# Optimization experiments

Measured on AMD Instinct MI355X. Metric: run time of the kernel, lower is better.

Reference implementation:

```python
import jax, jax.numpy as jnp
import numpy as np

TEMPERATURE = 0.07


def setup_inputs() -> dict:
    key = jax.random.key(0)
    k1, k2 = jax.random.split(key)
    B, D = 8192, 1024
    emb1 = jax.random.normal(k1, (B, D), dtype=jnp.float32)
    emb2 = jax.random.normal(k2, (B, D), dtype=jnp.float32)
    return {"emb1": emb1, "emb2": emb2}


def reference(emb1, emb2):
    B = emb1.shape[0]
    # [B, B] similarity logits scaled by temperature
    logits = jnp.matmul(emb1, emb2.T) / TEMPERATURE
    # SigLIP-style contrastive loss: diagonal entries are positives,
    # off-diagonal entries are negatives.
    # positive: -logsigmoid(logits) on diag; negative: -logsigmoid(-logits) off-diag
    pos = -jax.nn.log_sigmoid(jnp.diagonal(logits))            # [B]
    neg = -jax.nn.log_sigmoid(-logits)                          # [B, B]
    # negative_mask zeroes the diagonal -> subtract diagonal contribution
    neg_sum = neg.sum() - jnp.sum(jnp.diagonal(neg))
    loss = (pos.sum() + neg_sum) / B
    return loss
```

## Files before the change

### kernel.cpp

```cpp
#include <hip/hip_runtime.h>


#define B_DIM 8192
#define K_DIM 1024
#define BM 256
#define BN 128
#define BKB 128
#define NT (K_DIM / BKB)
#define ABRICK 32768
#define BBRICK 16384
#define BUFSZ 49152

typedef int i32x4 __attribute__((ext_vector_type(4)));
typedef int i32x8 __attribute__((ext_vector_type(8)));
typedef float f32x4 __attribute__((ext_vector_type(4)));

template <int PANEL>
__device__ __forceinline__ void brick_store(const float* __restrict__ in,
                                            unsigned char* __restrict__ out,
                                            float scale, int i) {
  constexpr int BRICK = PANEL * 128;
  const int o = i * 16;
  const int b = o / BRICK;
  const int p = b >> 3, t = b & 7;
  const int w = o & (BRICK - 1);
  const int fb = w >> 11;
  const int h = (w >> 10) & 1;
  const int kch = (w >> 8) & 3;
  const int lr = (w >> 4) & 15;
  const int row = p * PANEL + fb * 16 + lr;
  const int kb = t * 128 + kch * 32 + h * 16;
  const float4* src = (const float4*)(in + (size_t)row * K_DIM + kb);
  float4 v0 = src[0], v1 = src[1], v2 = src[2], v3 = src[3];
  unsigned w0 = 0, w1 = 0, w2 = 0, w3 = 0;
  w0 = __builtin_amdgcn_cvt_pk_fp8_f32(v0.x * scale, v0.y * scale, w0, 0);
  w0 = __builtin_amdgcn_cvt_pk_fp8_f32(v0.z * scale, v0.w * scale, w0, 1);
  w1 = __builtin_amdgcn_cvt_pk_fp8_f32(v1.x * scale, v1.y * scale, w1, 0);
  w1 = __builtin_amdgcn_cvt_pk_fp8_f32(v1.z * scale, v1.w * scale, w1, 1);
  w2 = __builtin_amdgcn_cvt_pk_fp8_f32(v2.x * scale, v2.y * scale, w2, 0);
  w2 = __builtin_amdgcn_cvt_pk_fp8_f32(v2.z * scale, v2.w * scale, w2, 1);
  w3 = __builtin_amdgcn_cvt_pk_fp8_f32(v3.x * scale, v3.y * scale, w3, 0);
  w3 = __builtin_amdgcn_cvt_pk_fp8_f32(v3.z * scale, v3.w * scale, w3, 1);
  *(uint4*)(out + o) = make_uint4(w0, w1, w2, w3);
}

__global__ __launch_bounds__(256) void cvt_fused(
    const float* __restrict__ e1, const float* __restrict__ e2,
    unsigned char* __restrict__ A8, unsigned char* __restrict__ B8,
    int nbA, float scaleA) {
  const int blk = blockIdx.x;
  if (blk < nbA)
    brick_store<BM>(e1, A8, scaleA, blk * 256 + threadIdx.x);
  else
    brick_store<BN>(e2, B8, 1.0f, (blk - nbA) * 256 + threadIdx.x);
}

template <bool DIAG>
__device__ __forceinline__ float softplus_sum(const f32x4 (&acc)[4][4],
                                              int rbase, int cbase) {
  float lin = 0.f, cor = 0.f;
#pragma unroll
  for (int m = 0; m < 4; ++m) {
#pragma unroll
    for (int n = 0; n < 4; ++n) {
#pragma unroll
      for (int r = 0; r < 4; ++r) {
        float x = acc[m][n][r];
        if (DIAG) {
          int row = rbase + m * 16 + r;
          int col = cbase + n * 16;
          if (row == col) x = -x;
        }
        lin += fmaxf(x, 0.f);
        cor += __logf(1.f + __expf(-fabsf(x)));
      }
    }
  }
  return lin + cor;
}

#define STAGEA(SB, J, TI)                                                     \
  __builtin_amdgcn_global_load_lds(                                           \
      (const __attribute__((address_space(1))) void*)(const void*)(           \
          srcA + (TI) * ABRICK + (J) * 8192),                                 \
      (__attribute__((address_space(3))) void*)(void*)(                       \
          lds + (SB) + dA + (J) * 8192),                                      \
      16, 0, 0)
#define STAGEB(SB, J, TI)                                                     \
  __builtin_amdgcn_global_load_lds(                                           \
      (const __attribute__((address_space(1))) void*)(const void*)(           \
          srcB + (TI) * BBRICK + (J) * 8192),                                 \
      (__attribute__((address_space(3))) void*)(void*)(                       \
          lds + (SB) + dB + (J) * 8192),                                      \
      16, 0, 0)

#define LDA(OUT, RB, M)                                                       \
  {                                                                           \
    const unsigned char* _b =                                                 \
        ldsL + ((RB) + ((wr * 4 + (M)) << 11));                               \
    i32x4 _lo = *(const i32x4*)(_b);                                          \
    i32x4 _hi = *(const i32x4*)(_b + 1024);                                   \
    OUT = __builtin_shufflevector(_lo, _hi, 0, 1, 2, 3, 4, 5, 6, 7);          \
  }
#define LDB(OUT, RB, N)                                                       \
  {                                                                           \
    const unsigned char* _b =                                                 \
        ldsL + ((RB) + 32768 + ((wc * 4 + (N)) << 11));                       \
    i32x4 _lo = *(const i32x4*)(_b);                                          \
    i32x4 _hi = *(const i32x4*)(_b + 1024);                                   \
    OUT = __builtin_shufflevector(_lo, _hi, 0, 1, 2, 3, 4, 5, 6, 7);          \
  }

#define MFMA(AF, BF, M, N)                                                    \
  acc[M][N] = __builtin_amdgcn_mfma_scale_f32_16x16x128_f8f6f4(               \
      AF, BF, acc[M][N], 0, 0, 0, 127, 0, 127)

__global__ __launch_bounds__(512, 1) void siglip_gemm(
    const unsigned char* __restrict__ A8,
    const unsigned char* __restrict__ B8,
    float* __restrict__ partials) {
  __shared__ unsigned char lds[3 * BUFSZ];
  __shared__ float wsum[8];

  const int tid = threadIdx.x;
  const int wave = tid >> 6;
  const int lane = tid & 63;
  const int wr = wave >> 1;
  const int wc = wave & 1;
  const int brow = blockIdx.y;
  const int bcol = blockIdx.x;

  f32x4 acc[4][4];
#pragma unroll
  for (int m = 0; m < 4; ++m)
#pragma unroll
    for (int n = 0; n < 4; ++n) acc[m][n] = f32x4{0.f, 0.f, 0.f, 0.f};

  const unsigned char* srcA =
      A8 + (size_t)brow * (NT * ABRICK) + wave * 1024 + (lane << 4);
  const unsigned char* srcB =
      B8 + (size_t)bcol * (NT * BBRICK) + wave * 1024 + (lane << 4);
  const int dA = wave * 1024;
  const int dB = 32768 + wave * 1024;
  const unsigned char* ldsL = lds + (lane << 4);

  STAGEA(0, 0, 0); STAGEA(0, 1, 0); STAGEA(0, 2, 0); STAGEA(0, 3, 0);
  STAGEB(0, 0, 0); STAGEB(0, 1, 0);
  STAGEA(BUFSZ, 0, 1); STAGEA(BUFSZ, 1, 1);
  STAGEA(BUFSZ, 2, 1); STAGEA(BUFSZ, 3, 1);
  STAGEB(BUFSZ, 0, 1); STAGEB(BUFSZ, 1, 1);
  asm volatile("s_waitcnt vmcnt(6)" ::: "memory");
  __builtin_amdgcn_s_barrier();
  __builtin_amdgcn_sched_barrier(0);

#pragma unroll
  for (int T = 0; T < NT; ++T) {
    const int rb = (T % 3) * BUFSZ;
    const int sb = ((T + 2) % 3) * BUFSZ;

    i32x8 b0, b1, b2, b3, a0, a1, a2, a3;
    LDB(b0, rb, 0); LDB(b1, rb, 1); LDB(b2, rb, 2); LDB(b3, rb, 3);
    LDA(a0, rb, 0); LDA(a1, rb, 1); LDA(a2, rb, 2); LDA(a3, rb, 3);

    if (T < NT - 2) {
      STAGEA(sb, 0, T + 2); STAGEA(sb, 1, T + 2);
      STAGEA(sb, 2, T + 2); STAGEA(sb, 3, T + 2);
      STAGEB(sb, 0, T + 2); STAGEB(sb, 1, T + 2);
      asm volatile("s_waitcnt vmcnt(6)" ::: "memory");
    } else if (T == NT - 2) {
      asm volatile("s_waitcnt vmcnt(0)" ::: "memory");
    }

    __builtin_amdgcn_s_setprio(1);
    MFMA(a0, b0, 0, 0); MFMA(a0, b1, 0, 1); MFMA(a0, b2, 0, 2); MFMA(a0, b3, 0, 3);
    MFMA(a1, b0, 1, 0); MFMA(a1, b1, 1, 1); MFMA(a1, b2, 1, 2); MFMA(a1, b3, 1, 3);
    MFMA(a2, b0, 2, 0); MFMA(a2, b1, 2, 1); MFMA(a2, b2, 2, 2); MFMA(a2, b3, 2, 3);
    MFMA(a3, b0, 3, 0); MFMA(a3, b1, 3, 1); MFMA(a3, b2, 3, 2); MFMA(a3, b3, 3, 3);
    __builtin_amdgcn_s_setprio(0);

    __builtin_amdgcn_s_barrier();
    __builtin_amdgcn_sched_barrier(0);
  }

  const int rbase = brow * BM + wr * 64 + (lane >> 4) * 4;
  const int cbase = bcol * BN + wc * 64 + (lane & 15);
  float lsum;
  if ((bcol >> 1) == brow)
    lsum = softplus_sum<true>(acc, rbase, cbase);
  else
    lsum = softplus_sum<false>(acc, rbase, cbase);

#pragma unroll
  for (int off = 32; off > 0; off >>= 1) lsum += __shfl_down(lsum, off);
  if (lane == 0) wsum[wave] = lsum;
  __syncthreads();
  if (tid == 0) {
    float s = 0.f;
#pragma unroll
    for (int w = 0; w < 8; ++w) s += wsum[w];
    partials[blockIdx.y * gridDim.x + blockIdx.x] = s;
  }
}

__global__ void reduce_kernel(const float* __restrict__ partials, int n,
                              float* __restrict__ out) {
  __shared__ float s[256];
  float v = 0.f;
  for (int i = threadIdx.x; i < n; i += 256) v += partials[i];
  s[threadIdx.x] = v;
  __syncthreads();
  for (int off = 128; off > 0; off >>= 1) {
    if ((int)threadIdx.x < off) s[threadIdx.x] += s[threadIdx.x + off];
    __syncthreads();
  }
  if (threadIdx.x == 0) out[0] = s[0] / (float)B_DIM;
}

extern "C" void kernel_launch(void* const* d_in, const int* in_sizes, int n_in,
                              void* d_out, int out_size, void* d_ws, size_t ws_size,
                              hipStream_t stream) {
  const float* emb1 = (const float*)d_in[0];
  const float* emb2 = (const float*)d_in[1];

  unsigned char* A8 = (unsigned char*)d_ws;
  unsigned char* B8 = A8 + (size_t)B_DIM * K_DIM;
  float* partials = (float*)(B8 + (size_t)B_DIM * K_DIM);

  const float INV_T = 1.0f / 0.07f;
  const int nbA = (B_DIM * K_DIM / 16) / 256;
  cvt_fused<<<2 * nbA, 256, 0, stream>>>(emb1, emb2, A8, B8, nbA, INV_T);

  dim3 grid(B_DIM / BN, B_DIM / BM);
  siglip_gemm<<<grid, 512, 0, stream>>>(A8, B8, partials);

  const int nparts = (B_DIM / BM) * (B_DIM / BN);
  reduce_kernel<<<1, 256, 0, stream>>>(partials, nparts, (float*)d_out);
}
```

Before: 119.5 us.

## Switch GEMM to 128x128 tiles, 4 waves, double buffering, two blocks per CU

Shrinks the GEMM block tile from 256x128 with 8 waves and triple-buffered LDS to 128x128 with 4 waves and double-buffered LDS, so two blocks can share a CU. The FP8 brick layout for both operands becomes a single 128-row panel. The aim is to overlap one block's memory waits with another block's compute instead of relying on a deeper per-block prefetch. In exchange, each A byte is loaded from global memory twice as often, the prefetch depth drops to one stage with a full vmcnt(0) wait every iteration, and the grid and partials count double.

```diff
diff --git a/kernel.cpp b/kernel.cpp
--- a/kernel.cpp
+++ b/kernel.cpp
@@ -3,32 +3,29 @@
 
 #define B_DIM 8192
 #define K_DIM 1024
-#define BM 256
-#define BN 128
+#define BT 128
 #define BKB 128
 #define NT (K_DIM / BKB)
-#define ABRICK 32768
-#define BBRICK 16384
-#define BUFSZ 49152
+#define BRICK 16384
+#define PANEL_BYTES (NT * BRICK)
+#define BUFSZ 32768
 
 typedef int i32x4 __attribute__((ext_vector_type(4)));
 typedef int i32x8 __attribute__((ext_vector_type(8)));
 typedef float f32x4 __attribute__((ext_vector_type(4)));
 
-template <int PANEL>
 __device__ __forceinline__ void brick_store(const float* __restrict__ in,
                                             unsigned char* __restrict__ out,
                                             float scale, int i) {
-  constexpr int BRICK = PANEL * 128;
   const int o = i * 16;
-  const int b = o / BRICK;
+  const int b = o >> 14;
   const int p = b >> 3, t = b & 7;
   const int w = o & (BRICK - 1);
   const int fb = w >> 11;
   const int h = (w >> 10) & 1;
   const int kch = (w >> 8) & 3;
   const int lr = (w >> 4) & 15;
-  const int row = p * PANEL + fb * 16 + lr;
+  const int row = p * 128 + fb * 16 + lr;
   const int kb = t * 128 + kch * 32 + h * 16;
   const float4* src = (const float4*)(in + (size_t)row * K_DIM + kb);
   float4 v0 = src[0], v1 = src[1], v2 = src[2], v3 = src[3];
@@ -50,9 +47,9 @@
     int nbA, float scaleA) {
   const int blk = blockIdx.x;
   if (blk < nbA)
-    brick_store<BM>(e1, A8, scaleA, blk * 256 + threadIdx.x);
+    brick_store(e1, A8, scaleA, blk * 256 + threadIdx.x);
   else
-    brick_store<BN>(e2, B8, 1.0f, (blk - nbA) * 256 + threadIdx.x);
+    brick_store(e2, B8, 1.0f, (blk - nbA) * 256 + threadIdx.x);
 }
 
 template <bool DIAG>
@@ -79,33 +76,31 @@
   return lin + cor;
 }
 
-#define STAGEA(SB, J, TI)                                                     \
+#define STAGEA(SB, Q, TI)                                                     \
   __builtin_amdgcn_global_load_lds(                                           \
       (const __attribute__((address_space(1))) void*)(const void*)(           \
-          srcA + (TI) * ABRICK + (J) * 8192),                                 \
+          srcA + (TI) * BRICK + (Q) * 1024),                                  \
       (__attribute__((address_space(3))) void*)(void*)(                       \
-          lds + (SB) + dA + (J) * 8192),                                      \
+          lds + (SB) + dA + (Q) * 1024),                                      \
       16, 0, 0)
-#define STAGEB(SB, J, TI)                                                     \
+#define STAGEB(SB, Q, TI)                                                     \
   __builtin_amdgcn_global_load_lds(                                           \
       (const __attribute__((address_space(1))) void*)(const void*)(           \
-          srcB + (TI) * BBRICK + (J) * 8192),                                 \
+          srcB + (TI) * BRICK + (Q) * 1024),                                  \
       (__attribute__((address_space(3))) void*)(void*)(                       \
-          lds + (SB) + dB + (J) * 8192),                                      \
+          lds + (SB) + dB + (Q) * 1024),                                      \
       16, 0, 0)
 
 #define LDA(OUT, RB, M)                                                       \
   {                                                                           \
-    const unsigned char* _b =                                                 \
-        ldsL + ((RB) + ((wr * 4 + (M)) << 11));                               \
+    const unsigned char* _b = ldsL + ((RB) + ((wr * 4 + (M)) << 11));         \
     i32x4 _lo = *(const i32x4*)(_b);                                          \
     i32x4 _hi = *(const i32x4*)(_b + 1024);                                   \
     OUT = __builtin_shufflevector(_lo, _hi, 0, 1, 2, 3, 4, 5, 6, 7);          \
   }
 #define LDB(OUT, RB, N)                                                       \
   {                                                                           \
-    const unsigned char* _b =                                                 \
-        ldsL + ((RB) + 32768 + ((wc * 4 + (N)) << 11));                       \
+    const unsigned char* _b = ldsL + ((RB) + 16384 + ((wc * 4 + (N)) << 11)); \
     i32x4 _lo = *(const i32x4*)(_b);                                          \
     i32x4 _hi = *(const i32x4*)(_b + 1024);                                   \
     OUT = __builtin_shufflevector(_lo, _hi, 0, 1, 2, 3, 4, 5, 6, 7);          \
@@ -115,12 +110,12 @@
   acc[M][N] = __builtin_amdgcn_mfma_scale_f32_16x16x128_f8f6f4(               \
       AF, BF, acc[M][N], 0, 0, 0, 127, 0, 127)
 
-__global__ __launch_bounds__(512, 1) void siglip_gemm(
+__global__ __launch_bounds__(256, 2) void siglip_gemm(
     const unsigned char* __restrict__ A8,
     const unsigned char* __restrict__ B8,
     float* __restrict__ partials) {
-  __shared__ unsigned char lds[3 * BUFSZ];
-  __shared__ float wsum[8];
+  __shared__ unsigned char lds[2 * BUFSZ];
+  __shared__ float wsum[4];
 
   const int tid = threadIdx.x;
   const int wave = tid >> 6;
@@ -137,39 +132,35 @@
     for (int n = 0; n < 4; ++n) acc[m][n] = f32x4{0.f, 0.f, 0.f, 0.f};
 
   const unsigned char* srcA =
-      A8 + (size_t)brow * (NT * ABRICK) + wave * 1024 + (lane << 4);
+      A8 + (size_t)brow * PANEL_BYTES + wave * 4096 + (lane << 4);
   const unsigned char* srcB =
-      B8 + (size_t)bcol * (NT * BBRICK) + wave * 1024 + (lane << 4);
-  const int dA = wave * 1024;
-  const int dB = 32768 + wave * 1024;
+      B8 + (size_t)bcol * PANEL_BYTES + wave * 4096 + (lane << 4);
+  const int dA = wave * 4096;
+  const int dB = 16384 + wave * 4096;
   const unsigned char* ldsL = lds + (lane << 4);
 
   STAGEA(0, 0, 0); STAGEA(0, 1, 0); STAGEA(0, 2, 0); STAGEA(0, 3, 0);
-  STAGEB(0, 0, 0); STAGEB(0, 1, 0);
-  STAGEA(BUFSZ, 0, 1); STAGEA(BUFSZ, 1, 1);
-  STAGEA(BUFSZ, 2, 1); STAGEA(BUFSZ, 3, 1);
-  STAGEB(BUFSZ, 0, 1); STAGEB(BUFSZ, 1, 1);
-  asm volatile("s_waitcnt vmcnt(6)" ::: "memory");
+  STAGEB(0, 0, 0); STAGEB(0, 1, 0); STAGEB(0, 2, 0); STAGEB(0, 3, 0);
+  asm volatile("s_waitcnt vmcnt(0)" ::: "memory");
   __builtin_amdgcn_s_barrier();
   __builtin_amdgcn_sched_barrier(0);
 
 #pragma unroll
   for (int T = 0; T < NT; ++T) {
-    const int rb = (T % 3) * BUFSZ;
-    const int sb = ((T + 2) % 3) * BUFSZ;
+    const int rb = (T & 1) * BUFSZ;
+    const int sb = rb ^ BUFSZ;
 
     i32x8 b0, b1, b2, b3, a0, a1, a2, a3;
     LDB(b0, rb, 0); LDB(b1, rb, 1); LDB(b2, rb, 2); LDB(b3, rb, 3);
     LDA(a0, rb, 0); LDA(a1, rb, 1); LDA(a2, rb, 2); LDA(a3, rb, 3);
 
-    if (T < NT - 2) {
-      STAGEA(sb, 0, T + 2); STAGEA(sb, 1, T + 2);
-      STAGEA(sb, 2, T + 2); STAGEA(sb, 3, T + 2);
-      STAGEB(sb, 0, T + 2); STAGEB(sb, 1, T + 2);
-      asm volatile("s_waitcnt vmcnt(6)" ::: "memory");
-    } else if (T == NT - 2) {
-      asm volatile("s_waitcnt vmcnt(0)" ::: "memory");
+    if (T < NT - 1) {
+      STAGEA(sb, 0, T + 1); STAGEA(sb, 1, T + 1);
+      STAGEA(sb, 2, T + 1); STAGEA(sb, 3, T + 1);
+      STAGEB(sb, 0, T + 1); STAGEB(sb, 1, T + 1);
+      STAGEB(sb, 2, T + 1); STAGEB(sb, 3, T + 1);
     }
+    __builtin_amdgcn_sched_barrier(0);
 
     __builtin_amdgcn_s_setprio(1);
     MFMA(a0, b0, 0, 0); MFMA(a0, b1, 0, 1); MFMA(a0, b2, 0, 2); MFMA(a0, b3, 0, 3);
@@ -178,28 +169,29 @@
     MFMA(a3, b0, 3, 0); MFMA(a3, b1, 3, 1); MFMA(a3, b2, 3, 2); MFMA(a3, b3, 3, 3);
     __builtin_amdgcn_s_setprio(0);
 
-    __builtin_amdgcn_s_barrier();
-    __builtin_amdgcn_sched_barrier(0);
-  }
-
-  const int rbase = brow * BM + wr * 64 + (lane >> 4) * 4;
-  const int cbase = bcol * BN + wc * 64 + (lane & 15);
+    if (T < NT - 1) {
+      asm volatile("s_waitcnt vmcnt(0)" ::: "memory");
+      __builtin_amdgcn_s_barrier();
+      __builtin_amdgcn_sched_barrier(0);
+    }
+  }
+
+  const int rbase = brow * BT + wr * 64 + (lane >> 4) * 4;
+  const int cbase = bcol * BT + wc * 64 + (lane & 15);
   float lsum;
-  if ((bcol >> 1) == brow)
+  if (brow == bcol)
     lsum = softplus_sum<true>(acc, rbase, cbase);
   else
     lsum = softplus_sum<false>(acc, rbase, cbase);
 
 #pragma unroll
   for (int off = 32; off > 0; off >>= 1) lsum += __shfl_down(lsum, off);
+  __syncthreads();
   if (lane == 0) wsum[wave] = lsum;
   __syncthreads();
-  if (tid == 0) {
-    float s = 0.f;
-#pragma unroll
-    for (int w = 0; w < 8; ++w) s += wsum[w];
-    partials[blockIdx.y * gridDim.x + blockIdx.x] = s;
-  }
+  if (tid == 0)
+    partials[blockIdx.y * gridDim.x + blockIdx.x] =
+        wsum[0] + wsum[1] + wsum[2] + wsum[3];
 }
 
 __global__ void reduce_kernel(const float* __restrict__ partials, int n,
@@ -230,9 +222,9 @@
   const int nbA = (B_DIM * K_DIM / 16) / 256;
   cvt_fused<<<2 * nbA, 256, 0, stream>>>(emb1, emb2, A8, B8, nbA, INV_T);
 
-  dim3 grid(B_DIM / BN, B_DIM / BM);
-  siglip_gemm<<<grid, 512, 0, stream>>>(A8, B8, partials);
-
-  const int nparts = (B_DIM / BM) * (B_DIM / BN);
+  dim3 grid(B_DIM / BT, B_DIM / BT);
+  siglip_gemm<<<grid, 256, 0, stream>>>(A8, B8, partials);
+
+  const int nparts = (B_DIM / BT) * (B_DIM / BT);
   reduce_kernel<<<1, 256, 0, stream>>>(partials, nparts, (float*)d_out);
 }
```

Result: faster. 113.6 us (-5.0%).
